# Optimization experiments

Hardware: AMD Instinct MI355X
Metric: run time of the kernel (lower is better)

The kernel has to match this reference:

```python
import jax, jax.numpy as jnp
import numpy as np

B, H, S, D = 8, 12, 1024, 64

def setup_inputs() -> dict:
    key = jax.random.key(0)
    kq, kk, kv = jax.random.split(key, 3)
    q = jax.random.normal(kq, (B, H, S, D), dtype=jnp.float32)
    k = jax.random.normal(kk, (B, H, S, D), dtype=jnp.float32)
    v = jax.random.normal(kv, (B, H, S, D), dtype=jnp.float32)
    scale = 8  # sqrt(d_head)
    return {"q": q, "k": k, "v": v, "scale": scale}

def reference(q, k, v, scale):
    # scores: (B,H,S,S) = q @ k^T / scale, softmax over last axis
    scores = jnp.einsum('bhqd,bhkd->bhqk', q, k) / scale
    attention_score = jax.nn.softmax(scores, axis=-1)
    # context: (B,H,S,D)
    attention_context = jnp.einsum('bhqk,bhkd->bhqd', attention_score, v)
    return (attention_score, attention_context)
```

## Files before the change

kernel.cpp:

```cpp
#include <hip/hip_runtime.h>


#define SLEN 1024
#define DHEAD 64
#define NBH 96
#define QROWS 16

typedef __attribute__((ext_vector_type(4))) float f32x4;
typedef __attribute__((ext_vector_type(4))) __bf16 bf16x4;
typedef __attribute__((ext_vector_type(8))) __bf16 bf16x8;

union BF8 { bf16x8 v; bf16x4 h[2]; };

#define KB_ELEMS ((size_t)NBH * SLEN * DHEAD)
#define WS_BYTES (KB_ELEMS * 2 * 2)

__global__ __launch_bounds__(256)
void prepass(const float* __restrict__ Kp, const float* __restrict__ Vp,
             __bf16* __restrict__ Kb, __bf16* __restrict__ VTb) {
  __shared__ float tf[64][68];
  const int b = blockIdx.x, t = threadIdx.x;
  if (b < 1536) {
    const int bh = b >> 4, kc = b & 15;
    const float* Vg = Vp + ((size_t)bh * SLEN + (size_t)kc * 64) * DHEAD;
    #pragma unroll
    for (int i = 0; i < 4; ++i) {
      int r = i * 16 + (t >> 4), d0 = (t & 15) * 4;
      f32x4 v = *(const f32x4*)(Vg + (size_t)r * DHEAD + d0);
      #pragma unroll
      for (int j = 0; j < 4; ++j) tf[r][d0 + j] = v[j];
    }
    __syncthreads();
    const int d = t >> 2, k0 = (t & 3) * 16;
    __bf16* dst = VTb + ((size_t)bh * DHEAD + d) * SLEN + kc * 64 + k0;
    BF8 o0, o1;
    #pragma unroll
    for (int kk = 0; kk < 8; ++kk) {
      o0.v[kk] = (__bf16)tf[k0 + kk][d];
      o1.v[kk] = (__bf16)tf[k0 + 8 + kk][d];
    }
    *(bf16x8*)dst = o0.v;
    *(bf16x8*)(dst + 8) = o1.v;
  } else {
    const size_t base = (size_t)(b - 1536) * 4096;
    #pragma unroll
    for (int i = 0; i < 4; ++i) {
      size_t off = base + i * 1024 + t * 4;
      f32x4 v = *(const f32x4*)(Kp + off);
      bf16x4 o;
      #pragma unroll
      for (int j = 0; j < 4; ++j) o[j] = (__bf16)v[j];
      *(bf16x4*)(Kb + off) = o;
    }
  }
}

struct SMem {
  __bf16 qt[QROWS][80];
  float red_m[4][16];
  float red_s[4][16];
  float ctxr[4][QROWS][72];
};

template<bool STAGED>
__global__ __launch_bounds__(256, 4)
void attn_main(const float* __restrict__ Qp, const float* __restrict__ Kp,
               const float* __restrict__ Vp, const __bf16* __restrict__ Kb,
               const __bf16* __restrict__ VTb, const int* __restrict__ scale_p,
               float* __restrict__ out) {
  __shared__ SMem sm;
  const int tid  = threadIdx.x;
  const int w    = tid >> 6;
  const int lane = tid & 63;
  const int quad = lane >> 4;
  const int c16  = lane & 15;

  const int bid   = blockIdx.x;
  const int slot  = bid >> 3;
  const int bh    = (bid & 7) * 12 + (slot >> 6);
  const int qbase = (slot & 63) * QROWS;

  int siv = *scale_p;
  float fs = (siv >= 1 && siv <= (1 << 24)) ? (float)siv : __int_as_float(siv);
  const float inv_scale = 1.0f / fs;

  {
    int r = tid >> 4, d0 = (tid & 15) * 4;
    f32x4 qv = *(const f32x4*)(Qp + ((size_t)bh * SLEN + qbase + r) * DHEAD + d0);
    bf16x4 o;
    #pragma unroll
    for (int j = 0; j < 4; ++j) o[j] = (__bf16)(qv[j] * inv_scale);
    *(bf16x4*)&sm.qt[r][d0] = o;
  }
  __syncthreads();

  BF8 qf0, qf1;
  qf0.v = *(const bf16x8*)&sm.qt[c16][quad * 8];
  qf1.v = *(const bf16x8*)&sm.qt[c16][32 + quad * 8];

  f32x4 acc[16];
  {
    f32x4 z = {0.0f, 0.0f, 0.0f, 0.0f};
    #pragma unroll
    for (int mt = 0; mt < 16; ++mt) acc[mt] = z;
  }
  const __bf16* Kbbase = STAGED ? Kb + ((size_t)bh * SLEN + w * 256) * DHEAD : nullptr;
  const float*  Kfbase = Kp + ((size_t)bh * SLEN + (size_t)w * 256) * DHEAD;
  #pragma unroll
  for (int mt = 0; mt < 16; ++mt) {
    int row = mt * 16 + c16;
    bf16x8 a0, a1;
    if constexpr (STAGED) {
      a0 = *(const bf16x8*)(Kbbase + (size_t)row * DHEAD + quad * 8);
      a1 = *(const bf16x8*)(Kbbase + (size_t)row * DHEAD + 32 + quad * 8);
    } else {
      const float* kr = Kfbase + (size_t)row * DHEAD + quad * 8;
      f32x4 x0 = *(const f32x4*)(kr);
      f32x4 x1 = *(const f32x4*)(kr + 4);
      f32x4 y0 = *(const f32x4*)(kr + 32);
      f32x4 y1 = *(const f32x4*)(kr + 36);
      #pragma unroll
      for (int j = 0; j < 4; ++j) {
        a0[j] = (__bf16)x0[j]; a0[j + 4] = (__bf16)x1[j];
        a1[j] = (__bf16)y0[j]; a1[j + 4] = (__bf16)y1[j];
      }
    }
    acc[mt] = __builtin_amdgcn_mfma_f32_16x16x32_bf16(a0, qf0.v, acc[mt], 0, 0, 0);
    acc[mt] = __builtin_amdgcn_mfma_f32_16x16x32_bf16(a1, qf1.v, acc[mt], 0, 0, 0);
  }

  float m;
  {
    float a = fmaxf(fmaxf(acc[0][0], acc[0][1]), fmaxf(acc[0][2], acc[0][3]));
    #pragma unroll
    for (int mt = 1; mt < 16; ++mt) {
      float b2 = fmaxf(fmaxf(acc[mt][0], acc[mt][1]), fmaxf(acc[mt][2], acc[mt][3]));
      a = fmaxf(a, b2);
    }
    a = fmaxf(a, __shfl_xor(a, 16));
    a = fmaxf(a, __shfl_xor(a, 32));
    if (lane < 16) sm.red_m[w][c16] = a;
  }
  __syncthreads();
  m = fmaxf(fmaxf(sm.red_m[0][c16], sm.red_m[1][c16]),
            fmaxf(sm.red_m[2][c16], sm.red_m[3][c16]));

  float s = 0.0f;
  #pragma unroll
  for (int mt = 0; mt < 16; ++mt)
    #pragma unroll
    for (int j = 0; j < 4; ++j) {
      float e = __expf(acc[mt][j] - m);
      acc[mt][j] = e;
      s += e;
    }
  s += __shfl_xor(s, 16);
  s += __shfl_xor(s, 32);
  if (lane < 16) sm.red_s[w][c16] = s;
  __syncthreads();
  const float inv = 1.0f / (sm.red_s[0][c16] + sm.red_s[1][c16] +
                            sm.red_s[2][c16] + sm.red_s[3][c16]);

  float* orow = out + ((size_t)bh * SLEN + qbase + c16) * SLEN + w * 256;
  BF8 pf[8];
  #pragma unroll
  for (int mt = 0; mt < 16; ++mt) {
    f32x4 p;
    #pragma unroll
    for (int j = 0; j < 4; ++j) p[j] = acc[mt][j] * inv;
    *(f32x4*)(orow + mt * 16 + quad * 4) = p;
    #pragma unroll
    for (int j = 0; j < 4; ++j)
      pf[mt >> 1].v[(mt & 1) * 4 + j] = (__bf16)p[j];
  }

  f32x4 ctx[4];
  {
    f32x4 z = {0.0f, 0.0f, 0.0f, 0.0f};
    #pragma unroll
    for (int dt = 0; dt < 4; ++dt) ctx[dt] = z;
  }
  const __bf16* Vt = STAGED ? VTb + (size_t)bh * DHEAD * SLEN : nullptr;
  #pragma unroll
  for (int t8 = 0; t8 < 8; ++t8) {
    int k0 = w * 256 + t8 * 32 + quad * 4;
    #pragma unroll
    for (int dt = 0; dt < 4; ++dt) {
      BF8 b;
      if constexpr (STAGED) {
        const __bf16* vr = Vt + (size_t)(dt * 16 + c16) * SLEN + k0;
        b.h[0] = *(const bf16x4*)(vr);
        b.h[1] = *(const bf16x4*)(vr + 16);
      } else {
        #pragma unroll
        for (int j = 0; j < 8; ++j)
          b.v[j] = (__bf16)Vp[((size_t)bh * SLEN + k0 + (j & 3) + 16 * (j >> 2)) * DHEAD +
                              dt * 16 + c16];
      }
      ctx[dt] = __builtin_amdgcn_mfma_f32_16x16x32_bf16(pf[t8].v, b.v, ctx[dt], 0, 0, 0);
    }
  }

  #pragma unroll
  for (int dt = 0; dt < 4; ++dt)
    #pragma unroll
    for (int i = 0; i < 4; ++i)
      sm.ctxr[w][quad * 4 + i][dt * 16 + c16] = ctx[dt][i];
  __syncthreads();
  {
    int q = tid >> 4, d4 = (tid & 15) * 4;
    f32x4 r0 = *(const f32x4*)&sm.ctxr[0][q][d4];
    f32x4 r1 = *(const f32x4*)&sm.ctxr[1][q][d4];
    f32x4 r2 = *(const f32x4*)&sm.ctxr[2][q][d4];
    f32x4 r3 = *(const f32x4*)&sm.ctxr[3][q][d4];
    f32x4 o;
    #pragma unroll
    for (int j = 0; j < 4; ++j) o[j] = (r0[j] + r1[j]) + (r2[j] + r3[j]);
    float* outC = out + (size_t)NBH * SLEN * SLEN;
    *(f32x4*)(outC + ((size_t)bh * SLEN + qbase + q) * DHEAD + d4) = o;
  }
}

extern "C" void kernel_launch(void* const* d_in, const int* in_sizes, int n_in,
                              void* d_out, int out_size, void* d_ws, size_t ws_size,
                              hipStream_t stream) {
  (void)in_sizes; (void)n_in; (void)out_size;
  const float* q = (const float*)d_in[0];
  const float* k = (const float*)d_in[1];
  const float* v = (const float*)d_in[2];
  const int* scale = (const int*)d_in[3];
  float* out = (float*)d_out;

  const bool staged = (d_ws != nullptr) && (ws_size >= (size_t)WS_BYTES);
  dim3 block(256);
  if (staged) {
    __bf16* Kb  = (__bf16*)d_ws;
    __bf16* VTb = Kb + KB_ELEMS;
    hipLaunchKernelGGL(prepass, dim3(3072), block, 0, stream, k, v, Kb, VTb);
    hipLaunchKernelGGL(attn_main<true>, dim3((SLEN / QROWS) * NBH), block, 0, stream,
                       q, k, v, Kb, VTb, scale, out);
  } else {
    hipLaunchKernelGGL(attn_main<false>, dim3((SLEN / QROWS) * NBH), block, 0, stream,
                       q, k, v, (const __bf16*)nullptr, (const __bf16*)nullptr, scale, out);
  }
}
```

Measured before the change: 718.7 us.

## Stage softmax probabilities through LDS for coalesced row stores; permute V^T layout

```diff
diff --git a/kernel.cpp b/kernel.cpp
--- a/kernel.cpp
+++ b/kernel.cpp
@@ -14,6 +14,10 @@
 
 #define KB_ELEMS ((size_t)NBH * SLEN * DHEAD)
 #define WS_BYTES (KB_ELEMS * 2 * 2)
+
+__device__ __forceinline__ int keyof(int tau) {
+  return 32 * (tau >> 5) + ((tau >> 3) & 3) * 4 + 16 * ((tau >> 2) & 1) + (tau & 3);
+}
 
 __global__ __launch_bounds__(256)
 void prepass(const float* __restrict__ Kp, const float* __restrict__ Vp,
@@ -31,13 +35,13 @@
       for (int j = 0; j < 4; ++j) tf[r][d0 + j] = v[j];
     }
     __syncthreads();
-    const int d = t >> 2, k0 = (t & 3) * 16;
-    __bf16* dst = VTb + ((size_t)bh * DHEAD + d) * SLEN + kc * 64 + k0;
+    const int d = t >> 2, tb = (t & 3) * 16;
+    __bf16* dst = VTb + ((size_t)bh * DHEAD + d) * SLEN + kc * 64 + tb;
     BF8 o0, o1;
     #pragma unroll
-    for (int kk = 0; kk < 8; ++kk) {
-      o0.v[kk] = (__bf16)tf[k0 + kk][d];
-      o1.v[kk] = (__bf16)tf[k0 + 8 + kk][d];
+    for (int x = 0; x < 8; ++x) {
+      o0.v[x] = (__bf16)tf[keyof(tb + x)][d];
+      o1.v[x] = (__bf16)tf[keyof(tb + 8 + x)][d];
     }
     *(bf16x8*)dst = o0.v;
     *(bf16x8*)(dst + 8) = o1.v;
@@ -59,7 +63,10 @@
   __bf16 qt[QROWS][80];
   float red_m[4][16];
   float red_s[4][16];
-  float ctxr[4][QROWS][72];
+  union {
+    float ctxr[4][QROWS][72];
+    float plin[2][QROWS][268];
+  } u;
 };
 
 template<bool STAGED>
@@ -161,17 +168,15 @@
   const float inv = 1.0f / (sm.red_s[0][c16] + sm.red_s[1][c16] +
                             sm.red_s[2][c16] + sm.red_s[3][c16]);
 
-  float* orow = out + ((size_t)bh * SLEN + qbase + c16) * SLEN + w * 256;
   BF8 pf[8];
   #pragma unroll
   for (int mt = 0; mt < 16; ++mt) {
-    f32x4 p;
-    #pragma unroll
-    for (int j = 0; j < 4; ++j) p[j] = acc[mt][j] * inv;
-    *(f32x4*)(orow + mt * 16 + quad * 4) = p;
-    #pragma unroll
-    for (int j = 0; j < 4; ++j)
-      pf[mt >> 1].v[(mt & 1) * 4 + j] = (__bf16)p[j];
+    #pragma unroll
+    for (int j = 0; j < 4; ++j) {
+      float p = acc[mt][j] * inv;
+      acc[mt][j] = p;
+      pf[mt >> 1].v[(mt & 1) * 4 + j] = (__bf16)p;
+    }
   }
 
   f32x4 ctx[4];
@@ -183,15 +188,14 @@
   const __bf16* Vt = STAGED ? VTb + (size_t)bh * DHEAD * SLEN : nullptr;
   #pragma unroll
   for (int t8 = 0; t8 < 8; ++t8) {
-    int k0 = w * 256 + t8 * 32 + quad * 4;
     #pragma unroll
     for (int dt = 0; dt < 4; ++dt) {
       BF8 b;
       if constexpr (STAGED) {
-        const __bf16* vr = Vt + (size_t)(dt * 16 + c16) * SLEN + k0;
-        b.h[0] = *(const bf16x4*)(vr);
-        b.h[1] = *(const bf16x4*)(vr + 16);
+        b.v = *(const bf16x8*)(Vt + (size_t)(dt * 16 + c16) * SLEN +
+                               w * 256 + t8 * 32 + quad * 8);
       } else {
+        int k0 = w * 256 + t8 * 32 + quad * 4;
         #pragma unroll
         for (int j = 0; j < 8; ++j)
           b.v[j] = (__bf16)Vp[((size_t)bh * SLEN + k0 + (j & 3) + 16 * (j >> 2)) * DHEAD +
@@ -205,19 +209,39 @@
   for (int dt = 0; dt < 4; ++dt)
     #pragma unroll
     for (int i = 0; i < 4; ++i)
-      sm.ctxr[w][quad * 4 + i][dt * 16 + c16] = ctx[dt][i];
+      sm.u.ctxr[w][quad * 4 + i][dt * 16 + c16] = ctx[dt][i];
   __syncthreads();
   {
     int q = tid >> 4, d4 = (tid & 15) * 4;
-    f32x4 r0 = *(const f32x4*)&sm.ctxr[0][q][d4];
-    f32x4 r1 = *(const f32x4*)&sm.ctxr[1][q][d4];
-    f32x4 r2 = *(const f32x4*)&sm.ctxr[2][q][d4];
-    f32x4 r3 = *(const f32x4*)&sm.ctxr[3][q][d4];
+    f32x4 r0 = *(const f32x4*)&sm.u.ctxr[0][q][d4];
+    f32x4 r1 = *(const f32x4*)&sm.u.ctxr[1][q][d4];
+    f32x4 r2 = *(const f32x4*)&sm.u.ctxr[2][q][d4];
+    f32x4 r3 = *(const f32x4*)&sm.u.ctxr[3][q][d4];
     f32x4 o;
     #pragma unroll
     for (int j = 0; j < 4; ++j) o[j] = (r0[j] + r1[j]) + (r2[j] + r3[j]);
     float* outC = out + (size_t)NBH * SLEN * SLEN;
     *(f32x4*)(outC + ((size_t)bh * SLEN + qbase + q) * DHEAD + d4) = o;
+  }
+  __syncthreads();
+
+  #pragma unroll
+  for (int r = 0; r < 2; ++r) {
+    if ((w >> 1) == r) {
+      #pragma unroll
+      for (int mt = 0; mt < 16; ++mt)
+        *(f32x4*)&sm.u.plin[w & 1][c16][mt * 16 + quad * 4] = acc[mt];
+    }
+    __syncthreads();
+    #pragma unroll
+    for (int jj = 0; jj < 8; ++jj) {
+      int idx = w * 8 + jj;
+      int h = idx >> 4, row = idx & 15;
+      f32x4 vls = *(const f32x4*)&sm.u.plin[h][row][lane * 4];
+      *(f32x4*)(out + ((size_t)bh * SLEN + qbase + row) * SLEN +
+                (size_t)(r * 2 + h) * 256 + lane * 4) = vls;
+    }
+    if (r == 0) __syncthreads();
   }
 }
 
```

Result: faster. 634.5 us (-11.7%).
